# Kernel tuning notes

Hardware: AMD Instinct MI355X
Metric: run time of the kernel (lower is better)

Reference implementation:

```python
import jax, jax.numpy as jnp
import numpy as np

MEM_SIZE = 65536
H = 128
T_DIM = 128
INP_DIM = 256
B = 2048


def setup_inputs() -> dict:
    key = jax.random.key(0)
    ks = jax.random.split(key, 8)
    return {
        "ts": jax.random.uniform(ks[0], (B,), dtype=jnp.float32) * 100.0,
        "inp": jax.random.normal(ks[1], (B, INP_DIM), dtype=jnp.float32),
        "memory": jax.random.normal(ks[2], (MEM_SIZE, H), dtype=jnp.float32),
        "w_t": jax.random.normal(ks[3], (T_DIM,), dtype=jnp.float32),
        "b_t": jax.random.normal(ks[4], (T_DIM,), dtype=jnp.float32),
        "Wq": jax.random.normal(ks[5], (H, T_DIM), dtype=jnp.float32) / np.sqrt(T_DIM),
        "Wk": jax.random.normal(ks[6], (H, H), dtype=jnp.float32) / np.sqrt(H),
        "Wv": jax.random.normal(ks[7], (H, INP_DIM), dtype=jnp.float32) / np.sqrt(INP_DIM),
    }


def _time_encode(t, w_t, b_t):
    # TGN-style cosine time encoding: [B] -> [B, T_DIM]
    return jnp.cos(t[:, None] * w_t[None, :] + b_t[None, :])


def reference(ts, inp, memory, w_t, b_t, Wq, Wk, Wv):
    # --- MemoryNet.update(ts, inp) ---
    t_emb = _time_encode(ts, w_t, b_t)            # [B, T_DIM]
    q_h = t_emb @ Wq.T                            # [B, H]
    k_h = memory @ Wk.T                           # [M, H]
    w = jax.nn.softmax(q_h @ k_h.T, axis=1)       # [B, M]
    v_h = inp @ Wv.T                              # [B, H]
    # (weight.unsqueeze(2) * v_h.unsqueeze(1)).sum(0) == w.T @ v_h, no [B,M,H] blowup
    new_mem = memory + jnp.einsum("bm,bh->mh", w, v_h)  # [M, H]
    # F.normalize(p=2, dim=1) with torch eps=1e-12
    norm = jnp.sqrt(jnp.sum(new_mem * new_mem, axis=1, keepdims=True))
    mem = new_mem / jnp.maximum(norm, 1e-12)

    # --- MemoryNet.forward(ts, mem): scaled attention read ---
    k2 = mem @ Wk.T                               # [M, H]
    scale = 1.0 / jnp.sqrt(jnp.asarray(H, dtype=mem.dtype))
    w2 = jax.nn.softmax((q_h @ k2.T) * scale, axis=1)  # [B, M]
    read_r = w2 @ mem                             # [B, H]
    return read_r
```

## Files before the change

### kernel.cpp

```cpp
#include <hip/hip_runtime.h>
#include <math.h>

#define B 2048
#define M 65536
#define H 128
#define TDIM 128
#define IDIM 256
#define SC 32
#define SCALE2 0.08838834764831845f
#define PST 36

typedef short bf8 __attribute__((ext_vector_type(8)));
typedef float f32x4 __attribute__((ext_vector_type(4)));
#define MFMA __builtin_amdgcn_mfma_f32_16x16x32_bf16
typedef unsigned short us;

#define SBAR() do { __builtin_amdgcn_sched_barrier(0); \
                    __builtin_amdgcn_s_barrier(); \
                    __builtin_amdgcn_sched_barrier(0); } while (0)
#define VMWAIT(N) do { asm volatile("s_waitcnt vmcnt(" #N ")" ::: "memory"); \
                       __builtin_amdgcn_sched_barrier(0); } while (0)
#define SCHED_FENCE() __builtin_amdgcn_sched_barrier(0)

__device__ inline us f2bf(float x) {
    unsigned u = __float_as_uint(x);
    u += 0x7FFF + ((u >> 16) & 1);
    return (us)(u >> 16);
}
__device__ inline float bf2f(us h) { return __uint_as_float(((unsigned)h) << 16); }
__device__ inline void split2(float x, us* hi, us* lo) {
    us h = f2bf(x); *hi = h; *lo = f2bf(x - bf2f(h));
}
__device__ inline void split2t(float x, us* hi, us* lo) {
    us h = (us)(__float_as_uint(x) >> 16);
    *hi = h; *lo = f2bf(x - bf2f(h));
}
__device__ inline bf8 ldb(const us* p) { return *(const bf8*)p; }
__device__ inline void gload16(const void* g, void* l) {
    __builtin_amdgcn_global_load_lds(
        (const __attribute__((address_space(1))) unsigned int*)g,
        (__attribute__((address_space(3))) unsigned int*)l, 16, 0, 0);
}

__global__ __launch_bounds__(128) void k_prep(const float* __restrict__ ts,
        const float* __restrict__ inp, const float* __restrict__ w_t,
        const float* __restrict__ b_t, const float* __restrict__ Wq,
        const float* __restrict__ Wk, const float* __restrict__ Wv,
        us* __restrict__ qt_hi, us* __restrict__ qt_lo, float* __restrict__ vh) {
    __shared__ float temb[TDIM];
    __shared__ float qh[H];
    const int b = blockIdx.x, t = threadIdx.x;
    temb[t] = cosf(ts[b] * w_t[t] + b_t[t]);
    __syncthreads();
    float s = 0.f;
    for (int k = 0; k < TDIM; k++) s += temb[k] * Wq[t * TDIM + k];
    qh[t] = s;
    __syncthreads();
    float s2 = 0.f;
    for (int j = 0; j < H; j++) s2 += qh[j] * Wk[j * H + t];
    us h, l;
    split2(s2, &h, &l);
    qt_hi[b * H + t] = h; qt_lo[b * H + t] = l;
    float s3 = 0.f;
    for (int i = 0; i < IDIM; i++) s3 += inp[b * IDIM + i] * Wv[t * IDIM + i];
    vh[b * H + t] = s3;
}

__global__ __launch_bounds__(256) void k_splitmem(const float* __restrict__ x,
        us* __restrict__ hi, us* __restrict__ lo, int n) {
    int i = blockIdx.x * 256 + threadIdx.x;
    const int stride = gridDim.x * 256;
    for (; i < n; i += stride) {
        us h, l;
        split2(x[i], &h, &l);
        hi[i] = h; lo[i] = l;
    }
}

__global__ __launch_bounds__(256) void k_tx(const float* __restrict__ vh,
        us* __restrict__ vhT_hi) {
    const int d = blockIdx.x;
    const int b = blockIdx.y * 256 + threadIdx.x;
    vhT_hi[d * B + b] = f2bf(vh[b * H + d]);
}

__global__ __launch_bounds__(256) void k_stats(const us* __restrict__ src_hi,
        const us* __restrict__ src_lo,
        const us* __restrict__ qt_hi, const us* __restrict__ qt_lo,
        int mchunk, float* __restrict__ pmax, float* __restrict__ psum) {
    __shared__ us lds[16384];
    const int tid = threadIdx.x;
    const int w = tid >> 6, l = tid & 63;
    const int lr = l & 15, g = l >> 4;
    const int brow = blockIdx.x * 128 + w * 32;
    const int m0b = blockIdx.y * mchunk;
    const int rq = l >> 4, cq = l & 15;
    bf8 qh[2][4], ql[2][4];
#pragma unroll
    for (int bt = 0; bt < 2; bt++)
#pragma unroll
        for (int kk = 0; kk < 4; kk++) {
            const int o = (brow + bt * 16 + lr) * H + kk * 32 + g * 8;
            qh[bt][kk] = ldb(qt_hi + o);
            ql[bt][kk] = ldb(qt_lo + o);
        }
    float mb[8], sm[8];
#pragma unroll
    for (int i = 0; i < 8; i++) { mb[i] = -INFINITY; sm[i] = 0.f; }
    auto STAGE = [&](int t, int bi) {
        const int m0 = m0b + t * 32;
        us* Q = lds + bi * 8192;
#pragma unroll
        for (int i = 0; i < 4; i++) {
            const int id = w * 4 + i;
            const int ii = id & 7;
            const int r = ii * 4 + rq;
            const int cc = cq ^ (r & 7);
            gload16((id < 8 ? src_hi : src_lo) + (size_t)(m0 + r) * H + cc * 8,
                    Q + (id < 8 ? 0 : 4096) + ii * 512);
        }
    };
    STAGE(0, 0);
    int cur = 0;
    const int NT = mchunk / 32;
    for (int t = 0; t < NT; t++) {
        if (t + 1 < NT) { STAGE(t + 1, cur ^ 1); VMWAIT(4); }
        else { VMWAIT(0); }
        SBAR();
        const us* Q = lds + cur * 8192;
        f32x4 c[2][2];
#pragma unroll
        for (int bt = 0; bt < 2; bt++)
#pragma unroll
            for (int mt = 0; mt < 2; mt++) c[bt][mt] = (f32x4){0.f, 0.f, 0.f, 0.f};
#pragma unroll
        for (int kk = 0; kk < 4; kk++) {
            const int co = ((kk * 4 + g) ^ (lr & 7)) * 8;
            bf8 b0h = *(const bf8*)(Q + lr * 128 + co);
            bf8 b0l = *(const bf8*)(Q + 4096 + lr * 128 + co);
            bf8 b1h = *(const bf8*)(Q + (16 + lr) * 128 + co);
            bf8 b1l = *(const bf8*)(Q + 4096 + (16 + lr) * 128 + co);
            c[0][0] = MFMA(qh[0][kk], b0h, c[0][0], 0, 0, 0);
            c[0][0] = MFMA(ql[0][kk], b0h, c[0][0], 0, 0, 0);
            c[0][0] = MFMA(qh[0][kk], b0l, c[0][0], 0, 0, 0);
            c[0][1] = MFMA(qh[0][kk], b1h, c[0][1], 0, 0, 0);
            c[0][1] = MFMA(ql[0][kk], b1h, c[0][1], 0, 0, 0);
            c[0][1] = MFMA(qh[0][kk], b1l, c[0][1], 0, 0, 0);
            c[1][0] = MFMA(qh[1][kk], b0h, c[1][0], 0, 0, 0);
            c[1][0] = MFMA(ql[1][kk], b0h, c[1][0], 0, 0, 0);
            c[1][0] = MFMA(qh[1][kk], b0l, c[1][0], 0, 0, 0);
            c[1][1] = MFMA(qh[1][kk], b1h, c[1][1], 0, 0, 0);
            c[1][1] = MFMA(ql[1][kk], b1h, c[1][1], 0, 0, 0);
            c[1][1] = MFMA(qh[1][kk], b1l, c[1][1], 0, 0, 0);
        }
        float dm = -INFINITY;
#pragma unroll
        for (int bt = 0; bt < 2; bt++)
#pragma unroll
            for (int mt = 0; mt < 2; mt++)
#pragma unroll
                for (int r = 0; r < 4; r++)
                    dm = fmaxf(dm, c[bt][mt][r] - mb[bt * 4 + r]);
        if (__any(dm > 8.f)) {
#pragma unroll
            for (int bt = 0; bt < 2; bt++)
#pragma unroll
                for (int r = 0; r < 4; r++) {
                    const int s = bt * 4 + r;
                    float mx = fmaxf(mb[s], fmaxf(c[bt][0][r], c[bt][1][r]));
                    sm[s] = sm[s] * __expf(mb[s] - mx)
                          + __expf(c[bt][0][r] - mx) + __expf(c[bt][1][r] - mx);
                    mb[s] = mx;
                }
        } else {
#pragma unroll
            for (int bt = 0; bt < 2; bt++)
#pragma unroll
                for (int r = 0; r < 4; r++) {
                    const int s = bt * 4 + r;
                    sm[s] += __expf(c[bt][0][r] - mb[s]) + __expf(c[bt][1][r] - mb[s]);
                }
        }
        if (t + 1 < NT) SBAR();
        cur ^= 1;
    }
#pragma unroll
    for (int s = 0; s < 8; s++) {
#pragma unroll
        for (int x = 1; x < 16; x <<= 1) {
            float om = __shfl_xor(mb[s], x);
            float os = __shfl_xor(sm[s], x);
            float nm = fmaxf(mb[s], om);
            sm[s] = sm[s] * __expf(mb[s] - nm) + os * __expf(om - nm);
            mb[s] = nm;
        }
    }
    if (lr == 0) {
#pragma unroll
        for (int bt = 0; bt < 2; bt++)
#pragma unroll
            for (int r = 0; r < 4; r++) {
                const int row = brow + bt * 16 + g * 4 + r;
                pmax[row * SC + blockIdx.y] = mb[bt * 4 + r];
                psum[row * SC + blockIdx.y] = sm[bt * 4 + r];
            }
    }
}

__global__ __launch_bounds__(256) void k_combine1(const float* __restrict__ pmax,
        const float* __restrict__ psum, float* __restrict__ ffac) {
    const int b = blockIdx.x * 256 + threadIdx.x;
    float mx = -INFINITY;
    for (int c = 0; c < SC; c++) mx = fmaxf(mx, pmax[b * SC + c]);
    float z = 0.f;
    for (int c = 0; c < SC; c++) z += psum[b * SC + c] * __expf(pmax[b * SC + c] - mx);
    ffac[b] = __expf(-mx) / z;
}

__global__ __launch_bounds__(512, 4) void k_update(const float* __restrict__ memory,
        const us* __restrict__ mem_hi, const us* __restrict__ mem_lo,
        const us* __restrict__ qt_hi, const us* __restrict__ qt_lo,
        const us* __restrict__ vhT_hi, const float* __restrict__ ffac,
        us* __restrict__ memw_hi, us* __restrict__ memw_lo,
        us* __restrict__ memwT_hi) {
    __shared__ us lds[29696];
    const int tid = threadIdx.x;
    const int w = tid >> 6, l = tid & 63;
    const int lr = l & 15, g = l >> 4;
    const int mrow = blockIdx.x * 128 + w * 16;
    const int rq = l >> 4, cq = l & 15;
    const int rv = l >> 2, cv = l & 3;
    bf8 bh[4], bl[4];
#pragma unroll
    for (int kk = 0; kk < 4; kk++) {
        const int o = (mrow + lr) * H + kk * 32 + g * 8;
        bh[kk] = ldb(mem_hi + o);
        bl[kk] = ldb(mem_lo + o);
    }
    f32x4 acc[8];
#pragma unroll
    for (int dt = 0; dt < 8; dt++) acc[dt] = (f32x4){0.f, 0.f, 0.f, 0.f};
    us* Ph = lds + 20480 + w * 1152;
    us* Pl = Ph + 576;
    auto STAGE_QT = [&](int t, int bi) {
        const int b0 = t * 32;
        us* Q = lds + bi * 8192;
#pragma unroll
        for (int i = 0; i < 2; i++) {
            const int id = w * 2 + i;
            const int ii = id & 7;
            const int r = ii * 4 + rq;
            const int cc = cq ^ (r & 7);
            gload16((id < 8 ? qt_hi : qt_lo) + (size_t)(b0 + r) * H + cc * 8,
                    Q + (id < 8 ? 0 : 4096) + ii * 512);
        }
    };
    auto STAGE_VH = [&](int t) {
        const int b0 = t * 32;
        us* V = lds + 16384;
        const int r = w * 16 + rv;
        const int cc = cv ^ ((rv >> 1) & 3);
        gload16(vhT_hi + (size_t)r * B + b0 + cc * 8, V + w * 512);
    };
    STAGE_QT(0, 0);
    STAGE_VH(0);
    int cur = 0;
    const int NT = B / 32;
    const us* V = lds + 16384;
    for (int t = 0; t < NT; t++) {
        const int b0 = t * 32;
        const float4 f4a = *(const float4*)(ffac + b0 + g * 4);
        const float4 f4b = *(const float4*)(ffac + b0 + 16 + g * 4);
        SCHED_FENCE();
        if (t + 1 < NT) { STAGE_QT(t + 1, cur ^ 1); SCHED_FENCE(); VMWAIT(5); }
        else { VMWAIT(3); }
        SBAR();
        const us* Q = lds + cur * 8192;
        f32x4 c[2];
        c[0] = (f32x4){0.f, 0.f, 0.f, 0.f};
        c[1] = (f32x4){0.f, 0.f, 0.f, 0.f};
#pragma unroll
        for (int kk = 0; kk < 4; kk++) {
            const int co = ((kk * 4 + g) ^ (lr & 7)) * 8;
            bf8 a0h = *(const bf8*)(Q + lr * 128 + co);
            bf8 a0l = *(const bf8*)(Q + 4096 + lr * 128 + co);
            bf8 a1h = *(const bf8*)(Q + (16 + lr) * 128 + co);
            bf8 a1l = *(const bf8*)(Q + 4096 + (16 + lr) * 128 + co);
            c[0] = MFMA(a0h, bh[kk], c[0], 0, 0, 0);
            c[0] = MFMA(a0l, bh[kk], c[0], 0, 0, 0);
            c[0] = MFMA(a0h, bl[kk], c[0], 0, 0, 0);
            c[1] = MFMA(a1h, bh[kk], c[1], 0, 0, 0);
            c[1] = MFMA(a1l, bh[kk], c[1], 0, 0, 0);
            c[1] = MFMA(a1h, bl[kk], c[1], 0, 0, 0);
        }
        const float fa[4] = {f4a.x, f4a.y, f4a.z, f4a.w};
        const float fb[4] = {f4b.x, f4b.y, f4b.z, f4b.w};
        const int ksw = 2 * (lr & 3);
#pragma unroll
        for (int bt = 0; bt < 2; bt++) {
            us hh[4], ll[4];
#pragma unroll
            for (int r = 0; r < 4; r++) {
                float p = __expf(c[bt][r]) * (bt ? fb[r] : fa[r]);
                split2t(p, &hh[r], &ll[r]);
            }
            uint2 v;
            v.x = (unsigned)hh[0] | ((unsigned)hh[1] << 16);
            v.y = (unsigned)hh[2] | ((unsigned)hh[3] << 16);
            const int so = lr * PST + ((bt * 4 + g) ^ ksw) * 4;
            *(uint2*)(Ph + so) = v;
            v.x = (unsigned)ll[0] | ((unsigned)ll[1] << 16);
            v.y = (unsigned)ll[2] | ((unsigned)ll[3] << 16);
            *(uint2*)(Pl + so) = v;
        }
        const int ro = lr * PST + (g ^ (lr & 3)) * 8;
        bf8 pah = *(const bf8*)(Ph + ro);
        bf8 pal = *(const bf8*)(Pl + ro);
        SBAR();
#pragma unroll
        for (int dt = 0; dt < 8; dt++) {
            bf8 vhh = *(const bf8*)(V + (dt * 16 + lr) * 32
                                      + ((g ^ ((lr >> 1) & 3)) * 8));
            acc[dt] = MFMA(pah, vhh, acc[dt], 0, 0, 0);
            acc[dt] = MFMA(pal, vhh, acc[dt], 0, 0, 0);
        }
        if (t + 1 < NT) {
            SBAR();
            STAGE_VH(t + 1);
        }
        cur ^= 1;
    }
    float n2[4] = {0.f, 0.f, 0.f, 0.f};
#pragma unroll
    for (int dt = 0; dt < 8; dt++)
#pragma unroll
        for (int r = 0; r < 4; r++) {
            float v = acc[dt][r]
                    + memory[(mrow + g * 4 + r) * H + dt * 16 + lr];
            acc[dt][r] = v;
            n2[r] += v * v;
        }
#pragma unroll
    for (int r = 0; r < 4; r++) {
#pragma unroll
        for (int x = 1; x < 16; x <<= 1) n2[r] += __shfl_xor(n2[r], x);
        n2[r] = 1.f / fmaxf(sqrtf(n2[r]), 1e-12f);
    }
#pragma unroll
    for (int dt = 0; dt < 8; dt++)
#pragma unroll
        for (int r = 0; r < 4; r++) {
            float vv = acc[dt][r] * n2[r];
            us h, lo2;
            split2t(vv, &h, &lo2);
            memw_hi[(mrow + g * 4 + r) * H + dt * 16 + lr] = h;
            memw_lo[(mrow + g * 4 + r) * H + dt * 16 + lr] = lo2;
        }
    __syncthreads();
#pragma unroll
    for (int dt = 0; dt < 8; dt++)
#pragma unroll
        for (int r = 0; r < 4; r++) {
            float vv = acc[dt][r] * n2[r];
            lds[(dt * 16 + lr) * 136 + w * 16 + g * 4 + r]
                = (us)(__float_as_uint(vv) >> 16);
        }
    __syncthreads();
    {
        const int d = tid >> 2, seg = tid & 3;
        uint4* dq = (uint4*)(memwT_hi + (size_t)d * M + blockIdx.x * 128 + seg * 32);
        const uint4* sp = (const uint4*)(lds + d * 136 + seg * 32);
#pragma unroll
        for (int j = 0; j < 4; j++) dq[j] = sp[j];
    }
}

__global__ __launch_bounds__(512, 4) void k_fread(const us* __restrict__ memw_hi,
        const us* __restrict__ memw_lo, const us* __restrict__ memwT_hi,
        const us* __restrict__ qt_hi, const us* __restrict__ qt_lo,
        float* __restrict__ part, float* __restrict__ pmax2,
        float* __restrict__ psum2, int mchunk) {
    __shared__ us lds[29696];
    const int tid = threadIdx.x;
    const int w = tid >> 6, l = tid & 63;
    const int lr = l & 15, g = l >> 4;
    const int brow = blockIdx.x * 128 + w * 16;
    const int m0b = blockIdx.y * mchunk;
    const int rq = l >> 4, cq = l & 15;
    const int rv = l >> 2, cv = l & 3;
    bf8 qh[4], ql[4];
#pragma unroll
    for (int kk = 0; kk < 4; kk++) {
        const int o = (brow + lr) * H + kk * 32 + g * 8;
        qh[kk] = ldb(qt_hi + o);
        ql[kk] = ldb(qt_lo + o);
    }
    f32x4 acc[8];
#pragma unroll
    for (int dt = 0; dt < 8; dt++) acc[dt] = (f32x4){0.f, 0.f, 0.f, 0.f};
    float mb0 = 0.f, sm0 = 0.f;
    us* Ph = lds + 20480 + w * 1152;
    us* Pl = Ph + 576;
    auto STAGE_MW = [&](int t, int bi) {
        const int m0 = m0b + t * 32;
        us* Q = lds + bi * 8192;
#pragma unroll
        for (int i = 0; i < 2; i++) {
            const int id = w * 2 + i;
            const int ii = id & 7;
            const int r = ii * 4 + rq;
            const int cc = cq ^ (r & 7);
            gload16((id < 8 ? memw_hi : memw_lo) + (size_t)(m0 + r) * H + cc * 8,
                    Q + (id < 8 ? 0 : 4096) + ii * 512);
        }
    };
    auto STAGE_WT = [&](int t) {
        const int m0 = m0b + t * 32;
        us* V = lds + 16384;
        const int r = w * 16 + rv;
        const int cc = cv ^ ((rv >> 1) & 3);
        gload16(memwT_hi + (size_t)r * M + m0 + cc * 8, V + w * 512);
    };
    STAGE_MW(0, 0);
    STAGE_WT(0);
    int cur = 0;
    const int NT = mchunk / 32;
    const us* V = lds + 16384;
    for (int t = 0; t < NT; t++) {
        if (t + 1 < NT) { STAGE_MW(t + 1, cur ^ 1); SCHED_FENCE(); VMWAIT(3); }
        else { VMWAIT(1); }
        SBAR();
        const us* Q = lds + cur * 8192;
        f32x4 c[2];
        c[0] = (f32x4){0.f, 0.f, 0.f, 0.f};
        c[1] = (f32x4){0.f, 0.f, 0.f, 0.f};
#pragma unroll
        for (int kk = 0; kk < 4; kk++) {
            const int co = ((kk * 4 + g) ^ (lr & 7)) * 8;
            bf8 a0h = *(const bf8*)(Q + lr * 128 + co);
            bf8 a0l = *(const bf8*)(Q + 4096 + lr * 128 + co);
            bf8 a1h = *(const bf8*)(Q + (16 + lr) * 128 + co);
            bf8 a1l = *(const bf8*)(Q + 4096 + (16 + lr) * 128 + co);
            c[0] = MFMA(a0h, qh[kk], c[0], 0, 0, 0);
            c[0] = MFMA(a0l, qh[kk], c[0], 0, 0, 0);
            c[0] = MFMA(a0h, ql[kk], c[0], 0, 0, 0);
            c[1] = MFMA(a1h, qh[kk], c[1], 0, 0, 0);
            c[1] = MFMA(a1l, qh[kk], c[1], 0, 0, 0);
            c[1] = MFMA(a1h, ql[kk], c[1], 0, 0, 0);
        }
        float s[2][4];
        float lmax = -INFINITY;
#pragma unroll
        for (int mt = 0; mt < 2; mt++)
#pragma unroll
            for (int r = 0; r < 4; r++) {
                s[mt][r] = c[mt][r] * SCALE2;
                lmax = fmaxf(lmax, s[mt][r]);
            }
        lmax = fmaxf(lmax, __shfl_xor(lmax, 16));
        lmax = fmaxf(lmax, __shfl_xor(lmax, 32));
        if (__any(lmax > mb0 + 8.f)) {
            float nm = fmaxf(mb0, lmax), f0 = __expf(mb0 - nm);
            sm0 *= f0;
            float fr[4];
#pragma unroll
            for (int r = 0; r < 4; r++) fr[r] = __shfl(f0, g * 4 + r);
#pragma unroll
            for (int dt = 0; dt < 8; dt++)
#pragma unroll
                for (int r = 0; r < 4; r++) acc[dt][r] *= fr[r];
            mb0 = nm;
        }
        const int ksw = 2 * (lr & 3);
#pragma unroll
        for (int mt = 0; mt < 2; mt++) {
            us hh[4], ll[4];
#pragma unroll
            for (int r = 0; r < 4; r++) {
                float p = __expf(s[mt][r] - mb0);
                sm0 += p;
                split2t(p, &hh[r], &ll[r]);
            }
            uint2 v;
            v.x = (unsigned)hh[0] | ((unsigned)hh[1] << 16);
            v.y = (unsigned)hh[2] | ((unsigned)hh[3] << 16);
            const int so = lr * PST + ((mt * 4 + g) ^ ksw) * 4;
            *(uint2*)(Ph + so) = v;
            v.x = (unsigned)ll[0] | ((unsigned)ll[1] << 16);
            v.y = (unsigned)ll[2] | ((unsigned)ll[3] << 16);
            *(uint2*)(Pl + so) = v;
        }
        const int ro = lr * PST + (g ^ (lr & 3)) * 8;
        bf8 pah = *(const bf8*)(Ph + ro);
        bf8 pal = *(const bf8*)(Pl + ro);
        if (t + 1 < NT) { VMWAIT(2); } else { VMWAIT(0); }
        SBAR();
#pragma unroll
        for (int dt = 0; dt < 8; dt++) {
            bf8 th = *(const bf8*)(V + (dt * 16 + lr) * 32
                                     + ((g ^ ((lr >> 1) & 3)) * 8));
            acc[dt] = MFMA(pah, th, acc[dt], 0, 0, 0);
            acc[dt] = MFMA(pal, th, acc[dt], 0, 0, 0);
        }
        if (t + 1 < NT) {
            SBAR();
            STAGE_WT(t + 1);
        }
        cur ^= 1;
    }
    sm0 += __shfl_xor(sm0, 16);
    sm0 += __shfl_xor(sm0, 32);
    if (g == 0) {
        pmax2[(size_t)blockIdx.y * B + brow + lr] = mb0;
        psum2[(size_t)blockIdx.y * B + brow + lr] = sm0;
    }
    float* rp = part + (size_t)blockIdx.y * B * H;
#pragma unroll
    for (int dt = 0; dt < 8; dt++)
#pragma unroll
        for (int r = 0; r < 4; r++)
            rp[(size_t)(brow + g * 4 + r) * H + dt * 16 + lr] = acc[dt][r];
}

__global__ __launch_bounds__(256) void k_fstats(const float* __restrict__ pmax2,
        const float* __restrict__ psum2, float* __restrict__ wc, int nc) {
    const int b = blockIdx.x * 256 + threadIdx.x;
    float gm = -INFINITY;
    for (int c = 0; c < nc; c++) gm = fmaxf(gm, pmax2[(size_t)c * B + b]);
    float z = 0.f;
    for (int c = 0; c < nc; c++)
        z += psum2[(size_t)c * B + b] * __expf(pmax2[(size_t)c * B + b] - gm);
    const float zi = 1.f / z;
    for (int c = 0; c < nc; c++)
        wc[(size_t)c * B + b] = __expf(pmax2[(size_t)c * B + b] - gm) * zi;
}

__global__ __launch_bounds__(256) void k_fcombine(const float* __restrict__ part,
        const float* __restrict__ wc, float* __restrict__ out, int nc) {
    const int i = blockIdx.x * 256 + threadIdx.x;
    const int b = i >> 7;
    float s = 0.f;
    for (int c = 0; c < nc; c++) s += part[(size_t)c * B * H + i] * wc[(size_t)c * B + b];
    out[i] = s;
}

extern "C" void kernel_launch(void* const* d_in, const int* in_sizes, int n_in,
                              void* d_out, int out_size, void* d_ws, size_t ws_size,
                              hipStream_t stream) {
    const float* ts     = (const float*)d_in[0];
    const float* inp    = (const float*)d_in[1];
    const float* memory = (const float*)d_in[2];
    const float* w_t    = (const float*)d_in[3];
    const float* b_t    = (const float*)d_in[4];
    const float* Wq     = (const float*)d_in[5];
    const float* Wk     = (const float*)d_in[6];
    const float* Wv     = (const float*)d_in[7];
    float* out = (float*)d_out;

    char* p = (char*)d_ws;
    auto alloc = [&](size_t bytes) { char* r = p; p += (bytes + 255) & ~(size_t)255; return r; };
    us* mem_hi   = (us*)alloc((size_t)M * H * 2);
    us* mem_lo   = (us*)alloc((size_t)M * H * 2);
    us* memw_hi  = (us*)alloc((size_t)M * H * 2);
    us* memw_lo  = (us*)alloc((size_t)M * H * 2);
    us* memwT_hi = (us*)alloc((size_t)M * H * 2);
    us* qt_hi    = (us*)alloc((size_t)B * H * 2);
    us* qt_lo    = (us*)alloc((size_t)B * H * 2);
    us* vhT_hi   = (us*)alloc((size_t)B * H * 2);
    float* vh    = (float*)alloc((size_t)B * H * 4);
    float* pmax  = (float*)alloc((size_t)B * SC * 4);
    float* psum  = (float*)alloc((size_t)B * SC * 4);
    float* ffac  = (float*)alloc((size_t)B * 4);
    size_t remain = ws_size - (size_t)(p - (char*)d_ws);
    int NC = 1;
    for (int c = 32; c >= 1; c >>= 1) {
        size_t need = (size_t)c * B * H * 4 + 3 * (size_t)c * B * 4 + 4096;
        if (need <= remain) { NC = c; break; }
    }
    float* pmax2 = (float*)alloc((size_t)NC * B * 4);
    float* psum2 = (float*)alloc((size_t)NC * B * 4);
    float* wcb   = (float*)alloc((size_t)NC * B * 4);
    float* part  = (float*)alloc((size_t)NC * B * H * 4);
    const int mchunk = M / NC;

    hipLaunchKernelGGL(k_prep, dim3(B), dim3(128), 0, stream,
                       ts, inp, w_t, b_t, Wq, Wk, Wv, qt_hi, qt_lo, vh);
    hipLaunchKernelGGL(k_splitmem, dim3(2048), dim3(256), 0, stream,
                       memory, mem_hi, mem_lo, M * H);
    hipLaunchKernelGGL(k_tx, dim3(H, B / 256), dim3(256), 0, stream, vh, vhT_hi);
    hipLaunchKernelGGL(k_stats, dim3(B / 128, SC), dim3(256), 0, stream,
                       mem_hi, mem_lo, qt_hi, qt_lo, M / SC, pmax, psum);
    hipLaunchKernelGGL(k_combine1, dim3(B / 256), dim3(256), 0, stream, pmax, psum, ffac);
    hipLaunchKernelGGL(k_update, dim3(M / 128), dim3(512), 0, stream,
                       memory, mem_hi, mem_lo, qt_hi, qt_lo, vhT_hi,
                       ffac, memw_hi, memw_lo, memwT_hi);
    hipLaunchKernelGGL(k_fread, dim3(B / 128, NC), dim3(512), 0, stream,
                       memw_hi, memw_lo, memwT_hi, qt_hi, qt_lo,
                       part, pmax2, psum2, mchunk);
    hipLaunchKernelGGL(k_fstats, dim3(B / 256), dim3(256), 0, stream, pmax2, psum2, wcb, NC);
    hipLaunchKernelGGL(k_fcombine, dim3(B * H / 256), dim3(256), 0, stream, part, wcb, out, NC);
}
```

Measured before the change: 574.0 us.

## Triple-buffer k_stats with 8 waves, drop P-tile barriers, add MFMA priority

k_stats moves from 4 waves of 32 batch rows to 8 waves of 16 rows and replaces its double buffer with a triple-buffered LDS ring, so the trailing barrier per tile can go. k_update and k_fread no longer place a barrier between the per-wave P tile writes and the PV MFMAs. They shrink the P stride from 36 to 32 and lower the vmcnt waits, and every MFMA block is wrapped in s_setprio. The intent is fewer barriers, more waves in flight, and less LDS use. The risks are LDS bank conflicts from the unpadded stride and hazards from the removed barriers and changed wait counts.

```diff
diff --git a/kernel.cpp b/kernel.cpp
--- a/kernel.cpp
+++ b/kernel.cpp
@@ -8,7 +8,7 @@
 #define IDIM 256
 #define SC 32
 #define SCALE2 0.08838834764831845f
-#define PST 36
+#define PST 32
 
 typedef short bf8 __attribute__((ext_vector_type(8)));
 typedef float f32x4 __attribute__((ext_vector_type(4)));
@@ -84,35 +84,33 @@
     vhT_hi[d * B + b] = f2bf(vh[b * H + d]);
 }
 
-__global__ __launch_bounds__(256) void k_stats(const us* __restrict__ src_hi,
+__global__ __launch_bounds__(512, 4) void k_stats(const us* __restrict__ src_hi,
         const us* __restrict__ src_lo,
         const us* __restrict__ qt_hi, const us* __restrict__ qt_lo,
         int mchunk, float* __restrict__ pmax, float* __restrict__ psum) {
-    __shared__ us lds[16384];
+    __shared__ us lds[24576];
     const int tid = threadIdx.x;
     const int w = tid >> 6, l = tid & 63;
     const int lr = l & 15, g = l >> 4;
-    const int brow = blockIdx.x * 128 + w * 32;
+    const int brow = blockIdx.x * 128 + w * 16;
     const int m0b = blockIdx.y * mchunk;
     const int rq = l >> 4, cq = l & 15;
-    bf8 qh[2][4], ql[2][4];
-#pragma unroll
-    for (int bt = 0; bt < 2; bt++)
-#pragma unroll
-        for (int kk = 0; kk < 4; kk++) {
-            const int o = (brow + bt * 16 + lr) * H + kk * 32 + g * 8;
-            qh[bt][kk] = ldb(qt_hi + o);
-            ql[bt][kk] = ldb(qt_lo + o);
-        }
-    float mb[8], sm[8];
-#pragma unroll
-    for (int i = 0; i < 8; i++) { mb[i] = -INFINITY; sm[i] = 0.f; }
+    bf8 qh[4], ql[4];
+#pragma unroll
+    for (int kk = 0; kk < 4; kk++) {
+        const int o = (brow + lr) * H + kk * 32 + g * 8;
+        qh[kk] = ldb(qt_hi + o);
+        ql[kk] = ldb(qt_lo + o);
+    }
+    float mb[4], sm[4];
+#pragma unroll
+    for (int i = 0; i < 4; i++) { mb[i] = -INFINITY; sm[i] = 0.f; }
     auto STAGE = [&](int t, int bi) {
         const int m0 = m0b + t * 32;
         us* Q = lds + bi * 8192;
 #pragma unroll
-        for (int i = 0; i < 4; i++) {
-            const int id = w * 4 + i;
+        for (int i = 0; i < 2; i++) {
+            const int id = w * 2 + i;
             const int ii = id & 7;
             const int r = ii * 4 + rq;
             const int cc = cq ^ (r & 7);
@@ -121,18 +119,18 @@
         }
     };
     STAGE(0, 0);
-    int cur = 0;
+    int qr = 0;
     const int NT = mchunk / 32;
     for (int t = 0; t < NT; t++) {
-        if (t + 1 < NT) { STAGE(t + 1, cur ^ 1); VMWAIT(4); }
+        const int nx = (qr == 2) ? 0 : qr + 1;
+        if (t + 1 < NT) { STAGE(t + 1, nx); VMWAIT(2); }
         else { VMWAIT(0); }
         SBAR();
-        const us* Q = lds + cur * 8192;
-        f32x4 c[2][2];
-#pragma unroll
-        for (int bt = 0; bt < 2; bt++)
-#pragma unroll
-            for (int mt = 0; mt < 2; mt++) c[bt][mt] = (f32x4){0.f, 0.f, 0.f, 0.f};
+        const us* Q = lds + qr * 8192;
+        f32x4 c[2];
+        c[0] = (f32x4){0.f, 0.f, 0.f, 0.f};
+        c[1] = (f32x4){0.f, 0.f, 0.f, 0.f};
+        __builtin_amdgcn_s_setprio(1);
 #pragma unroll
         for (int kk = 0; kk < 4; kk++) {
             const int co = ((kk * 4 + g) ^ (lr & 7)) * 8;
@@ -140,70 +138,53 @@
             bf8 b0l = *(const bf8*)(Q + 4096 + lr * 128 + co);
             bf8 b1h = *(const bf8*)(Q + (16 + lr) * 128 + co);
             bf8 b1l = *(const bf8*)(Q + 4096 + (16 + lr) * 128 + co);
-            c[0][0] = MFMA(qh[0][kk], b0h, c[0][0], 0, 0, 0);
-            c[0][0] = MFMA(ql[0][kk], b0h, c[0][0], 0, 0, 0);
-            c[0][0] = MFMA(qh[0][kk], b0l, c[0][0], 0, 0, 0);
-            c[0][1] = MFMA(qh[0][kk], b1h, c[0][1], 0, 0, 0);
-            c[0][1] = MFMA(ql[0][kk], b1h, c[0][1], 0, 0, 0);
-            c[0][1] = MFMA(qh[0][kk], b1l, c[0][1], 0, 0, 0);
-            c[1][0] = MFMA(qh[1][kk], b0h, c[1][0], 0, 0, 0);
-            c[1][0] = MFMA(ql[1][kk], b0h, c[1][0], 0, 0, 0);
-            c[1][0] = MFMA(qh[1][kk], b0l, c[1][0], 0, 0, 0);
-            c[1][1] = MFMA(qh[1][kk], b1h, c[1][1], 0, 0, 0);
-            c[1][1] = MFMA(ql[1][kk], b1h, c[1][1], 0, 0, 0);
-            c[1][1] = MFMA(qh[1][kk], b1l, c[1][1], 0, 0, 0);
-        }
+            c[0] = MFMA(qh[kk], b0h, c[0], 0, 0, 0);
+            c[0] = MFMA(ql[kk], b0h, c[0], 0, 0, 0);
+            c[0] = MFMA(qh[kk], b0l, c[0], 0, 0, 0);
+            c[1] = MFMA(qh[kk], b1h, c[1], 0, 0, 0);
+            c[1] = MFMA(ql[kk], b1h, c[1], 0, 0, 0);
+            c[1] = MFMA(qh[kk], b1l, c[1], 0, 0, 0);
+        }
+        __builtin_amdgcn_s_setprio(0);
         float dm = -INFINITY;
 #pragma unroll
-        for (int bt = 0; bt < 2; bt++)
-#pragma unroll
-            for (int mt = 0; mt < 2; mt++)
-#pragma unroll
-                for (int r = 0; r < 4; r++)
-                    dm = fmaxf(dm, c[bt][mt][r] - mb[bt * 4 + r]);
+        for (int mt = 0; mt < 2; mt++)
+#pragma unroll
+            for (int r = 0; r < 4; r++)
+                dm = fmaxf(dm, c[mt][r] - mb[r]);
         if (__any(dm > 8.f)) {
 #pragma unroll
-            for (int bt = 0; bt < 2; bt++)
-#pragma unroll
-                for (int r = 0; r < 4; r++) {
-                    const int s = bt * 4 + r;
-                    float mx = fmaxf(mb[s], fmaxf(c[bt][0][r], c[bt][1][r]));
-                    sm[s] = sm[s] * __expf(mb[s] - mx)
-                          + __expf(c[bt][0][r] - mx) + __expf(c[bt][1][r] - mx);
-                    mb[s] = mx;
-                }
+            for (int r = 0; r < 4; r++) {
+                float mx = fmaxf(mb[r], fmaxf(c[0][r], c[1][r]));
+                sm[r] = sm[r] * __expf(mb[r] - mx)
+                      + __expf(c[0][r] - mx) + __expf(c[1][r] - mx);
+                mb[r] = mx;
+            }
         } else {
 #pragma unroll
-            for (int bt = 0; bt < 2; bt++)
-#pragma unroll
-                for (int r = 0; r < 4; r++) {
-                    const int s = bt * 4 + r;
-                    sm[s] += __expf(c[bt][0][r] - mb[s]) + __expf(c[bt][1][r] - mb[s]);
-                }
-        }
-        if (t + 1 < NT) SBAR();
-        cur ^= 1;
-    }
-#pragma unroll
-    for (int s = 0; s < 8; s++) {
+            for (int r = 0; r < 4; r++)
+                sm[r] += __expf(c[0][r] - mb[r]) + __expf(c[1][r] - mb[r]);
+        }
+        qr = nx;
+    }
+#pragma unroll
+    for (int r = 0; r < 4; r++) {
 #pragma unroll
         for (int x = 1; x < 16; x <<= 1) {
-            float om = __shfl_xor(mb[s], x);
-            float os = __shfl_xor(sm[s], x);
-            float nm = fmaxf(mb[s], om);
-            sm[s] = sm[s] * __expf(mb[s] - nm) + os * __expf(om - nm);
-            mb[s] = nm;
+            float om = __shfl_xor(mb[r], x);
+            float os = __shfl_xor(sm[r], x);
+            float nm = fmaxf(mb[r], om);
+            sm[r] = sm[r] * __expf(mb[r] - nm) + os * __expf(om - nm);
+            mb[r] = nm;
         }
     }
     if (lr == 0) {
 #pragma unroll
-        for (int bt = 0; bt < 2; bt++)
-#pragma unroll
-            for (int r = 0; r < 4; r++) {
-                const int row = brow + bt * 16 + g * 4 + r;
-                pmax[row * SC + blockIdx.y] = mb[bt * 4 + r];
-                psum[row * SC + blockIdx.y] = sm[bt * 4 + r];
-            }
+        for (int r = 0; r < 4; r++) {
+            const int row = brow + g * 4 + r;
+            pmax[row * SC + blockIdx.y] = mb[r];
+            psum[row * SC + blockIdx.y] = sm[r];
+        }
     }
 }
 
@@ -223,7 +204,7 @@
         const us* __restrict__ vhT_hi, const float* __restrict__ ffac,
         us* __restrict__ memw_hi, us* __restrict__ memw_lo,
         us* __restrict__ memwT_hi) {
-    __shared__ us lds[29696];
+    __shared__ us lds[28672];
     const int tid = threadIdx.x;
     const int w = tid >> 6, l = tid & 63;
     const int lr = l & 15, g = l >> 4;
@@ -240,8 +221,8 @@
     f32x4 acc[8];
 #pragma unroll
     for (int dt = 0; dt < 8; dt++) acc[dt] = (f32x4){0.f, 0.f, 0.f, 0.f};
-    us* Ph = lds + 20480 + w * 1152;
-    us* Pl = Ph + 576;
+    us* Ph = lds + 20480 + w * 1024;
+    us* Pl = Ph + 512;
     auto STAGE_QT = [&](int t, int bi) {
         const int b0 = t * 32;
         us* Q = lds + bi * 8192;
@@ -272,13 +253,14 @@
         const float4 f4a = *(const float4*)(ffac + b0 + g * 4);
         const float4 f4b = *(const float4*)(ffac + b0 + 16 + g * 4);
         SCHED_FENCE();
-        if (t + 1 < NT) { STAGE_QT(t + 1, cur ^ 1); SCHED_FENCE(); VMWAIT(5); }
-        else { VMWAIT(3); }
+        if (t + 1 < NT) { STAGE_QT(t + 1, cur ^ 1); SCHED_FENCE(); VMWAIT(4); }
+        else { VMWAIT(2); }
         SBAR();
         const us* Q = lds + cur * 8192;
         f32x4 c[2];
         c[0] = (f32x4){0.f, 0.f, 0.f, 0.f};
         c[1] = (f32x4){0.f, 0.f, 0.f, 0.f};
+        __builtin_amdgcn_s_setprio(1);
 #pragma unroll
         for (int kk = 0; kk < 4; kk++) {
             const int co = ((kk * 4 + g) ^ (lr & 7)) * 8;
@@ -293,6 +275,7 @@
             c[1] = MFMA(a1l, bh[kk], c[1], 0, 0, 0);
             c[1] = MFMA(a1h, bl[kk], c[1], 0, 0, 0);
         }
+        __builtin_amdgcn_s_setprio(0);
         const float fa[4] = {f4a.x, f4a.y, f4a.z, f4a.w};
         const float fb[4] = {f4b.x, f4b.y, f4b.z, f4b.w};
         const int ksw = 2 * (lr & 3);
@@ -316,7 +299,7 @@
         const int ro = lr * PST + (g ^ (lr & 3)) * 8;
         bf8 pah = *(const bf8*)(Ph + ro);
         bf8 pal = *(const bf8*)(Pl + ro);
-        SBAR();
+        __builtin_amdgcn_s_setprio(1);
 #pragma unroll
         for (int dt = 0; dt < 8; dt++) {
             bf8 vhh = *(const bf8*)(V + (dt * 16 + lr) * 32
@@ -324,6 +307,7 @@
             acc[dt] = MFMA(pah, vhh, acc[dt], 0, 0, 0);
             acc[dt] = MFMA(pal, vhh, acc[dt], 0, 0, 0);
         }
+        __builtin_amdgcn_s_setprio(0);
         if (t + 1 < NT) {
             SBAR();
             STAGE_VH(t + 1);
@@ -380,7 +364,7 @@
         const us* __restrict__ qt_hi, const us* __restrict__ qt_lo,
         float* __restrict__ part, float* __restrict__ pmax2,
         float* __restrict__ psum2, int mchunk) {
-    __shared__ us lds[29696];
+    __shared__ us lds[28672];
     const int tid = threadIdx.x;
     const int w = tid >> 6, l = tid & 63;
     const int lr = l & 15, g = l >> 4;
@@ -399,8 +383,8 @@
 #pragma unroll
     for (int dt = 0; dt < 8; dt++) acc[dt] = (f32x4){0.f, 0.f, 0.f, 0.f};
     float mb0 = 0.f, sm0 = 0.f;
-    us* Ph = lds + 20480 + w * 1152;
-    us* Pl = Ph + 576;
+    us* Ph = lds + 20480 + w * 1024;
+    us* Pl = Ph + 512;
     auto STAGE_MW = [&](int t, int bi) {
         const int m0 = m0b + t * 32;
         us* Q = lds + bi * 8192;
@@ -427,13 +411,14 @@
     const int NT = mchunk / 32;
     const us* V = lds + 16384;
     for (int t = 0; t < NT; t++) {
-        if (t + 1 < NT) { STAGE_MW(t + 1, cur ^ 1); SCHED_FENCE(); VMWAIT(3); }
-        else { VMWAIT(1); }
+        if (t + 1 < NT) { STAGE_MW(t + 1, cur ^ 1); SCHED_FENCE(); VMWAIT(2); }
+        else { VMWAIT(0); }
         SBAR();
         const us* Q = lds + cur * 8192;
         f32x4 c[2];
         c[0] = (f32x4){0.f, 0.f, 0.f, 0.f};
         c[1] = (f32x4){0.f, 0.f, 0.f, 0.f};
+        __builtin_amdgcn_s_setprio(1);
 #pragma unroll
         for (int kk = 0; kk < 4; kk++) {
             const int co = ((kk * 4 + g) ^ (lr & 7)) * 8;
@@ -448,6 +433,7 @@
             c[1] = MFMA(a1l, qh[kk], c[1], 0, 0, 0);
             c[1] = MFMA(a1h, ql[kk], c[1], 0, 0, 0);
         }
+        __builtin_amdgcn_s_setprio(0);
         float s[2][4];
         float lmax = -INFINITY;
 #pragma unroll
@@ -493,8 +479,7 @@
         const int ro = lr * PST + (g ^ (lr & 3)) * 8;
         bf8 pah = *(const bf8*)(Ph + ro);
         bf8 pal = *(const bf8*)(Pl + ro);
-        if (t + 1 < NT) { VMWAIT(2); } else { VMWAIT(0); }
-        SBAR();
+        __builtin_amdgcn_s_setprio(1);
 #pragma unroll
         for (int dt = 0; dt < 8; dt++) {
             bf8 th = *(const bf8*)(V + (dt * 16 + lr) * 32
@@ -502,6 +487,7 @@
             acc[dt] = MFMA(pah, th, acc[dt], 0, 0, 0);
             acc[dt] = MFMA(pal, th, acc[dt], 0, 0, 0);
         }
+        __builtin_amdgcn_s_setprio(0);
         if (t + 1 < NT) {
             SBAR();
             STAGE_WT(t + 1);
@@ -588,7 +574,7 @@
     hipLaunchKernelGGL(k_splitmem, dim3(2048), dim3(256), 0, stream,
                        memory, mem_hi, mem_lo, M * H);
     hipLaunchKernelGGL(k_tx, dim3(H, B / 256), dim3(256), 0, stream, vh, vhT_hi);
-    hipLaunchKernelGGL(k_stats, dim3(B / 128, SC), dim3(256), 0, stream,
+    hipLaunchKernelGGL(k_stats, dim3(B / 128, SC), dim3(512), 0, stream,
                        mem_hi, mem_lo, qt_hi, qt_lo, M / SC, pmax, psum);
     hipLaunchKernelGGL(k_combine1, dim3(B / 256), dim3(256), 0, stream, pmax, psum, ffac);
     hipLaunchKernelGGL(k_update, dim3(M / 128), dim3(512), 0, stream,
```

New measurement: 528.8 us (median of 2 runs). 1.09x faster.
